# Kernel tuning notes

Hardware: AMD Instinct MI355X
Metric: run time of the kernel (lower is better)

Reference implementation:

```python
import jax, jax.numpy as jnp
import numpy as np

N = 100000       # nodes
E = 3200000      # edges
IN_DIM = 128
EDGE_DIM = 16
H = 64           # hidden_dim
L = 3            # num_layers
G = 256          # num graphs
BN_EPS = 1e-5


def setup_inputs() -> dict:
    key = jax.random.key(0)
    ks = jax.random.split(key, 16)
    x = jax.random.normal(ks[0], (N, IN_DIM), dtype=jnp.float32)
    edge_attr = jax.random.normal(ks[1], (E, EDGE_DIM), dtype=jnp.float32)
    edge_index = jax.random.randint(ks[2], (2, E), 0, N, dtype=jnp.int64)
    batch = jnp.sort(jax.random.randint(ks[3], (N,), 0, G, dtype=jnp.int64))
    s = 0.05
    np_w = jax.random.normal(ks[4], (IN_DIM, H), dtype=jnp.float32) * s
    np_b = jnp.zeros((H,), dtype=jnp.float32)
    ep_w = jax.random.normal(ks[5], (EDGE_DIM, H), dtype=jnp.float32) * s
    ep_b = jnp.zeros((H,), dtype=jnp.float32)
    mlp_w1 = jax.random.normal(ks[6], (L, H, H), dtype=jnp.float32) * s
    mlp_b1 = jnp.zeros((L, H), dtype=jnp.float32)
    mlp_w2 = jax.random.normal(ks[7], (L, H, H), dtype=jnp.float32) * s
    mlp_b2 = jnp.zeros((L, H), dtype=jnp.float32)
    bn_g = jnp.ones((L, H), dtype=jnp.float32)
    bn_b = jnp.zeros((L, H), dtype=jnp.float32)
    return {"x": x, "edge_attr": edge_attr, "edge_index": edge_index, "batch": batch,
            "np_w": np_w, "np_b": np_b, "ep_w": ep_w, "ep_b": ep_b,
            "mlp_w1": mlp_w1, "mlp_b1": mlp_b1, "mlp_w2": mlp_w2, "mlp_b2": mlp_b2,
            "bn_g": bn_g, "bn_b": bn_b}


def reference(x, edge_attr, edge_index, batch, np_w, np_b, ep_w, ep_b,
              mlp_w1, mlp_b1, mlp_w2, mlp_b2, bn_g, bn_b):
    h = x @ np_w + np_b                  # [N,H] node_proj
    e = edge_attr @ ep_w + ep_b          # [E,H] edge_proj
    src, dst = edge_index[0], edge_index[1]
    for l in range(L):
        # GINEConv (eps=0): MLP(x_i + sum_j ReLU(x_j + e_ij))
        msg = jax.nn.relu(h[src] + e)                          # [E,H] gather + edge add
        agg = jax.ops.segment_sum(msg, dst, num_segments=N)    # scatter-add
        z = h + agg
        z = jax.nn.relu(z @ mlp_w1[l] + mlp_b1[l]) @ mlp_w2[l] + mlp_b2[l]
        # BatchNorm1d over node dim (batch statistics, training-mode math)
        mu = jnp.mean(z, axis=0)
        var = jnp.mean((z - mu) ** 2, axis=0)
        z = (z - mu) * jax.lax.rsqrt(var + BN_EPS) * bn_g[l] + bn_b[l]
        h = jax.nn.relu(z)               # dropout omitted (deterministic reference)
    # global_mean_pool
    sums = jax.ops.segment_sum(h, batch, num_segments=G)
    cnts = jax.ops.segment_sum(jnp.ones((N,), dtype=h.dtype), batch, num_segments=G)
    graph_emb = sums / jnp.maximum(cnts, 1.0)[:, None]
    return h, graph_emb
```

## Files before the change

### kernel.cpp

```cpp
#include <hip/hip_runtime.h>
#include <hip/hip_bf16.h>

#define NN 100000
#define NE 3200000
#define IND 128
#define ED 16
#define HD 64
#define NL 3
#define NG 256
#define BN_EPS 1e-5f

#define NB 391
#define PBLK 512
#define PCHUNK 6250
#define MLP_BLOCKS 2048
#define APPLY_BLOCKS 2048

typedef unsigned int uint32;
typedef unsigned long long uint64;
typedef unsigned short ushort16;
typedef __attribute__((ext_vector_type(8))) short bf16x8;
typedef __attribute__((ext_vector_type(4))) float f32x4;

__device__ __forceinline__ ushort16 f2b(float f) {
    uint32 u = __float_as_uint(f);
    u = (u + 0x7fffu + ((u >> 16) & 1u)) >> 16;
    return (ushort16)u;
}
__device__ __forceinline__ float b2f(ushort16 b) {
    return __uint_as_float(((uint32)b) << 16);
}

__global__ __launch_bounds__(256) void k_node_proj(
    const float* __restrict__ x, const float* __restrict__ w,
    const float* __restrict__ b, ushort16* __restrict__ sb)
{
    __shared__ float xs[4][IND];
    const int wave = threadIdx.x >> 6, lane = threadIdx.x & 63;
    const int node = blockIdx.x * 4 + wave;
    const float2 v = *(const float2*)(x + (size_t)node * IND + lane * 2);
    ((float2*)xs[wave])[lane] = v;
    float acc = b[lane];
#pragma unroll
    for (int k = 0; k < IND; ++k)
        acc = fmaf(xs[wave][k], w[k * HD + lane], acc);
    sb[node * HD + lane] = f2b(acc);
}

__global__ __launch_bounds__(256) void k_p1(const int* __restrict__ ei,
                                            int* __restrict__ bh)
{
    __shared__ int hist[NB];
    const int t = threadIdx.x, blk = blockIdx.x;
    for (int i = t; i < NB; i += 256) hist[i] = 0;
    __syncthreads();
    const int base = blk * PCHUNK;
    for (int i = t; i < PCHUNK; i += 256)
        atomicAdd(&hist[ei[NE + base + i] >> 8], 1);
    __syncthreads();
    for (int i = t; i < NB; i += 256) bh[blk * NB + i] = hist[i];
}

__global__ __launch_bounds__(512) void k_p2(int* __restrict__ bh,
                                            int* __restrict__ bstart,
                                            int* __restrict__ rowptr)
{
    __shared__ int tot[NB];
    __shared__ int bsl[NB + 1];
    const int t = threadIdx.x;
    if (t < NB) {
        int s = 0;
        for (int blk = 0; blk < PBLK; ++blk) {
            const int idx = blk * NB + t;
            const int v = bh[idx];
            bh[idx] = s;
            s += v;
        }
        tot[t] = s;
    }
    __syncthreads();
    if (t == 0) {
        int run = 0;
        for (int b = 0; b < NB; ++b) { bsl[b] = run; run += tot[b]; }
        bsl[NB] = run;
    }
    __syncthreads();
    if (t < NB) {
        const int base = bsl[t];
        for (int blk = 0; blk < PBLK; ++blk) bh[blk * NB + t] += base;
        bstart[t] = base;
    }
    if (t == 0) { bstart[NB] = NE; rowptr[NN] = NE; }
}

__global__ __launch_bounds__(256) void k_p3(const int* __restrict__ ei,
                                            const int* __restrict__ bh,
                                            uint64* __restrict__ tmp)
{
    __shared__ int cursor[NB];
    const int t = threadIdx.x, blk = blockIdx.x;
    for (int i = t; i < NB; i += 256) cursor[i] = bh[blk * NB + i];
    __syncthreads();
    const int base = blk * PCHUNK;
    for (int i = t; i < PCHUNK; i += 256) {
        const int e = base + i;
        const int d = ei[NE + e];
        const int s = ei[e];
        const int pos = atomicAdd(&cursor[d >> 8], 1);
        tmp[pos] = (uint64)(uint32)d | ((uint64)(uint32)s << 17)
                 | ((uint64)(uint32)e << 34);
    }
}

__global__ __launch_bounds__(256) void k_p4(const uint64* __restrict__ tmp,
                                            const int* __restrict__ bstart,
                                            int* __restrict__ perm_src,
                                            int* __restrict__ perm_eid,
                                            int* __restrict__ rowptr)
{
    __shared__ int cnt[256], csave[256], cnt2[256];
    const int t = threadIdx.x, b = blockIdx.x;
    const int lo = bstart[b], hi = bstart[b + 1];
    cnt[t] = 0; cnt2[t] = 0;
    __syncthreads();
    for (int e = lo + t; e < hi; e += 256)
        atomicAdd(&cnt[(int)(tmp[e] & 0x1FFFF) & 255], 1);
    __syncthreads();
    csave[t] = cnt[t];
    __syncthreads();
    for (int off = 1; off < 256; off <<= 1) {
        const int v = (t >= off) ? cnt[t - off] : 0;
        __syncthreads();
        cnt[t] += v;
        __syncthreads();
    }
    const int excl = cnt[t] - csave[t];
    const int node = (b << 8) + t;
    if (node < NN) rowptr[node] = lo + excl;
    __syncthreads();
    csave[t] = excl;
    __syncthreads();
    for (int e = lo + t; e < hi; e += 256) {
        const uint64 u = tmp[e];
        const int loc = (int)(u & 0x1FFFF) & 255;
        const int r = atomicAdd(&cnt2[loc], 1);
        const int pos = lo + csave[loc] + r;
        perm_src[pos] = (int)((u >> 17) & 0x1FFFF);
        perm_eid[pos] = (int)(u >> 34);
    }
}

__global__ __launch_bounds__(256) void k_permute(
    const float* __restrict__ ea, const int* __restrict__ perm_eid,
    ushort16* __restrict__ ea_perm)
{
    const int pos = blockIdx.x * 256 + threadIdx.x;
    const int p = pos >> 2, q = pos & 3;
    const int eid = perm_eid[p];
    const float4 v = ((const float4*)(ea + (size_t)eid * ED))[q];
    ushort4 o;
    o.x = f2b(v.x); o.y = f2b(v.y); o.z = f2b(v.z); o.w = f2b(v.w);
    ((ushort4*)ea_perm)[pos] = o;
}

template <bool XFORM>
__global__ __launch_bounds__(256) void k_gather(
    const ushort16* __restrict__ eab, const int* __restrict__ perm_src,
    const int* __restrict__ rowptr,
    const float* __restrict__ epw, const float* __restrict__ epb,
    const ushort16* __restrict__ sb, const float* __restrict__ bnp,
    float* __restrict__ z)
{
    __shared__ float pe[4][64 * 17];
    const int lane = threadIdx.x & 63;
    const int wave = threadIdx.x >> 6;
    const int l15 = lane & 15, lg = lane >> 4;

    bf16x8 bfrag[4];
#pragma unroll
    for (int c = 0; c < 4; ++c) {
#pragma unroll
        for (int i = 0; i < 8; ++i) {
            const int k = lg * 8 + i;
            bfrag[c][i] = (k < ED) ? (short)f2b(epw[k * HD + c * 16 + l15])
                                   : (short)0;
        }
    }
    const float bc = epb[lane];
    const float tsc = XFORM ? bnp[lane] : 1.f;
    const float tsh = XFORM ? bnp[64 + lane] : 0.f;
    float* mype = pe[wave];

    const int node = __builtin_amdgcn_readfirstlane((blockIdx.x << 2) + wave);
    const int rs = rowptr[node];
    const int re = rowptr[node + 1];

    float acc = 0.f;
    for (int j = rs; j < re; j += 16) {
        bf16x8 a = {};
        if (lg < 2) {
            int row = j + l15;
            if (row > NE - 1) row = NE - 1;
            a = *(const bf16x8*)((const short*)eab + (size_t)row * ED + lg * 8);
        }
        const f32x4 zero = {0.f, 0.f, 0.f, 0.f};
#pragma unroll
        for (int c = 0; c < 4; ++c) {
            const f32x4 d = __builtin_amdgcn_mfma_f32_16x16x32_bf16(
                a, bfrag[c], zero, 0, 0, 0);
            const int base = (c * 16 + l15) * 17 + lg * 4;
#pragma unroll
            for (int v = 0; v < 4; ++v) mype[base + v] = d[v];
        }
#pragma unroll
        for (int half = 0; half < 2; ++half) {
            const int jb = j + half * 8;
            int s[8];
#pragma unroll
            for (int m = 0; m < 8; ++m) {
                int idx = jb + m;
                if (idx > NE - 1) idx = NE - 1;
                s[m] = perm_src[idx];
            }
            float hv[8];
#pragma unroll
            for (int m = 0; m < 8; ++m) {
                float v = b2f(sb[(size_t)s[m] * HD + lane]);
                if (XFORM) v = fmaxf(fmaf(v, tsc, tsh), 0.f);
                hv[m] = v;
            }
            const int lim = re - jb;
#pragma unroll
            for (int m = 0; m < 8; ++m) {
                if (m < lim) {
                    const float e = mype[lane * 17 + half * 8 + m] + bc;
                    acc += fmaxf(hv[m] + e, 0.f);
                }
            }
        }
    }
    float u0 = b2f(sb[(size_t)node * HD + lane]);
    if (XFORM) u0 = fmaxf(fmaf(u0, tsc, tsh), 0.f);
    z[node * HD + lane] = acc + u0;
}

template <bool STORE_BF16>
__global__ __launch_bounds__(256) void k_mlp(
    float* __restrict__ z,
    const float* __restrict__ w1, const float* __restrict__ b1,
    const float* __restrict__ w2, const float* __restrict__ b2,
    ushort16* __restrict__ sb, float* __restrict__ part)
{
    __shared__ float z0s[4][HD];
    __shared__ float t1s[4][HD];
    __shared__ float red[4][2][HD];
    const int wave = threadIdx.x >> 6, lane = threadIdx.x & 63;
    const float vb1 = b1[lane], vb2 = b2[lane];
    float s1 = 0.f, s2 = 0.f;
    for (int node = blockIdx.x * 4 + wave; node < NN; node += MLP_BLOCKS * 4) {
        const int idx = node * HD + lane;
        z0s[wave][lane] = z[idx];
        float a = vb1;
#pragma unroll
        for (int k = 0; k < HD; ++k)
            a = fmaf(z0s[wave][k], w1[k * HD + lane], a);
        a = fmaxf(a, 0.f);
        t1s[wave][lane] = a;
        float o = vb2;
#pragma unroll
        for (int k = 0; k < HD; ++k)
            o = fmaf(t1s[wave][k], w2[k * HD + lane], o);
        if (STORE_BF16) sb[idx] = f2b(o);
        else            z[idx] = o;
        s1 += o;
        s2 += o * o;
    }
    red[wave][0][lane] = s1;
    red[wave][1][lane] = s2;
    __syncthreads();
    if (wave == 0) {
        float a = red[0][0][lane] + red[1][0][lane] + red[2][0][lane] + red[3][0][lane];
        float c = red[0][1][lane] + red[1][1][lane] + red[2][1][lane] + red[3][1][lane];
        part[blockIdx.x * 128 + lane] = a;
        part[blockIdx.x * 128 + 64 + lane] = c;
    }
}

__global__ __launch_bounds__(1024) void k_bn_final(
    const float* __restrict__ part,
    const float* __restrict__ g, const float* __restrict__ b,
    float* __restrict__ bnp)
{
    __shared__ float red[16][2][HD];
    const int c = threadIdx.x & 63;
    const int s = threadIdx.x >> 6;
    float s1 = 0.f, s2 = 0.f;
    for (int i = s; i < MLP_BLOCKS; i += 16) {
        s1 += part[i * 128 + c];
        s2 += part[i * 128 + 64 + c];
    }
    red[s][0][c] = s1;
    red[s][1][c] = s2;
    __syncthreads();
    if (s == 0) {
        float a = 0.f, q = 0.f;
#pragma unroll
        for (int i = 0; i < 16; ++i) { a += red[i][0][c]; q += red[i][1][c]; }
        const float mu  = a / (float)NN;
        const float var = q / (float)NN - mu * mu;
        const float rstd = rsqrtf(var + BN_EPS);
        const float sc = rstd * g[c];
        bnp[c] = sc;
        bnp[64 + c] = b[c] - mu * sc;
    }
}

__global__ __launch_bounds__(256) void k_bn_apply(
    const float* __restrict__ t2, const float* __restrict__ bnp,
    float* __restrict__ h)
{
    const int lane = threadIdx.x & 63;
    const float sc = bnp[lane];
    const float sh = bnp[64 + lane];
    int i = blockIdx.x * 256 + threadIdx.x;
    const int stride = APPLY_BLOCKS * 256;
    for (; i < NN * HD; i += stride)
        h[i] = fmaxf(t2[i] * sc + sh, 0.f);
}

__global__ __launch_bounds__(256) void k_pool(
    const float* __restrict__ h, const int* __restrict__ batch,
    float* __restrict__ emb)
{
    __shared__ float red[4][HD];
    const int g = blockIdx.x;
    const int lane = threadIdx.x & 63;
    const int wave = threadIdx.x >> 6;
    int lo = 0, hi = NN;
    while (lo < hi) { int m = (lo + hi) >> 1; if (batch[m] < g) lo = m + 1; else hi = m; }
    const int start = lo;
    hi = NN;
    while (lo < hi) { int m = (lo + hi) >> 1; if (batch[m] <= g) lo = m + 1; else hi = m; }
    const int end = lo;
    float acc = 0.f;
    for (int n = start + wave; n < end; n += 4) acc += h[(size_t)n * HD + lane];
    red[wave][lane] = acc;
    __syncthreads();
    if (wave == 0) {
        float a = red[0][lane] + red[1][lane] + red[2][lane] + red[3][lane];
        emb[g * HD + lane] = a / fmaxf((float)(end - start), 1.f);
    }
}

extern "C" void kernel_launch(void* const* d_in, const int* in_sizes, int n_in,
                              void* d_out, int out_size, void* d_ws, size_t ws_size,
                              hipStream_t stream)
{
    const float* x     = (const float*)d_in[0];
    const float* ea    = (const float*)d_in[1];
    const int*   ei    = (const int*)d_in[2];
    const int*   batch = (const int*)d_in[3];
    const float* np_w  = (const float*)d_in[4];
    const float* np_b  = (const float*)d_in[5];
    const float* ep_w  = (const float*)d_in[6];
    const float* ep_b  = (const float*)d_in[7];
    const float* w1    = (const float*)d_in[8];
    const float* b1    = (const float*)d_in[9];
    const float* w2    = (const float*)d_in[10];
    const float* b2    = (const float*)d_in[11];
    const float* bng   = (const float*)d_in[12];
    const float* bnb   = (const float*)d_in[13];

    float* h   = (float*)d_out;
    float* emb = h + (size_t)NN * HD;

    char* ws = (char*)d_ws;
    float*     agg      = (float*)    (ws);
    uint64*    tmp      = (uint64*)   (ws);
    float*     part     = (float*)    (ws + 25600000);
    float*     bnp      = (float*)    (ws + 26648576);
    int*       bh       = (int*)      (ws + 26650112);
    int*       bstart   = (int*)      (ws + 27450880);
    int*       rowptr   = (int*)      (ws + 27452448);
    ushort16*  sb       = (ushort16*) (ws + 27852464);
    int*       perm_src = (int*)      (ws + 40652464);
    int*       perm_eid = (int*)      (ws + 53452464);
    ushort16*  ea_perm  = (ushort16*) (ws + 66252464);

    k_node_proj<<<NN / 4, 256, 0, stream>>>(x, np_w, np_b, sb);

    k_p1<<<PBLK, 256, 0, stream>>>(ei, bh);
    k_p2<<<1, 512, 0, stream>>>(bh, bstart, rowptr);
    k_p3<<<PBLK, 256, 0, stream>>>(ei, bh, tmp);
    k_p4<<<NB, 256, 0, stream>>>(tmp, bstart, perm_src, perm_eid, rowptr);
    k_permute<<<NE * 4 / 256, 256, 0, stream>>>(ea, perm_eid, ea_perm);

    for (int l = 0; l < NL; ++l) {
        if (l == 0)
            k_gather<false><<<NN / 4, 256, 0, stream>>>(
                ea_perm, perm_src, rowptr, ep_w, ep_b, sb, bnp, agg);
        else
            k_gather<true><<<NN / 4, 256, 0, stream>>>(
                ea_perm, perm_src, rowptr, ep_w, ep_b, sb, bnp + (l - 1) * 128, agg);
        if (l < NL - 1)
            k_mlp<true><<<MLP_BLOCKS, 256, 0, stream>>>(
                agg, w1 + l * HD * HD, b1 + l * HD, w2 + l * HD * HD, b2 + l * HD,
                sb, part);
        else
            k_mlp<false><<<MLP_BLOCKS, 256, 0, stream>>>(
                agg, w1 + l * HD * HD, b1 + l * HD, w2 + l * HD * HD, b2 + l * HD,
                sb, part);
        k_bn_final<<<1, 1024, 0, stream>>>(part, bng + l * HD, bnb + l * HD, bnp + l * 128);
    }

    k_bn_apply<<<APPLY_BLOCKS, 256, 0, stream>>>(agg, bnp + 2 * 128, h);
    k_pool<<<NG, 256, 0, stream>>>(h, batch, emb);
}
```

Baseline: 1.301 ms.

## Prefetch 16 neighbor gathers before MFMA and fold edge bias into matmul

In the gather kernel, all 16 source indices and neighbor features are now loaded up front, before the edge-projection MFMA, so the gather latency overlaps with the matrix work instead of being issued in two serialized halves. The edge bias is folded into the MFMA by adding a constant-one column to the A fragment and a bias row to the B fragment, which drops a per-edge add. MLP_BLOCKS is also reduced from 2048 to 512. Holding 16 gathered values live raises register pressure, and the bias is now rounded to bf16.

```diff
diff --git a/kernel.cpp b/kernel.cpp
--- a/kernel.cpp
+++ b/kernel.cpp
@@ -13,7 +13,7 @@
 #define NB 391
 #define PBLK 512
 #define PCHUNK 6250
-#define MLP_BLOCKS 2048
+#define MLP_BLOCKS 512
 #define APPLY_BLOCKS 2048
 
 typedef unsigned int uint32;
@@ -182,11 +182,12 @@
 #pragma unroll
         for (int i = 0; i < 8; ++i) {
             const int k = lg * 8 + i;
-            bfrag[c][i] = (k < ED) ? (short)f2b(epw[k * HD + c * 16 + l15])
-                                   : (short)0;
-        }
-    }
-    const float bc = epb[lane];
+            short v = 0;
+            if (k < ED)       v = (short)f2b(epw[k * HD + c * 16 + l15]);
+            else if (k == ED) v = (short)f2b(epb[c * 16 + l15]);
+            bfrag[c][i] = v;
+        }
+    }
     const float tsc = XFORM ? bnp[lane] : 1.f;
     const float tsh = XFORM ? bnp[64 + lane] : 0.f;
     float* mype = pe[wave];
@@ -197,12 +198,27 @@
 
     float acc = 0.f;
     for (int j = rs; j < re; j += 16) {
+        int s[16];
+#pragma unroll
+        for (int m = 0; m < 16; ++m) {
+            int idx = j + m;
+            if (idx > NE - 1) idx = NE - 1;
+            s[m] = perm_src[idx];
+        }
+        float hv[16];
+#pragma unroll
+        for (int m = 0; m < 16; ++m)
+            hv[m] = b2f(sb[(size_t)s[m] * HD + lane]);
+
         bf16x8 a = {};
         if (lg < 2) {
             int row = j + l15;
             if (row > NE - 1) row = NE - 1;
             a = *(const bf16x8*)((const short*)eab + (size_t)row * ED + lg * 8);
-        }
+        } else if (lg == 2) {
+            a[0] = (short)0x3F80;
+        }
+
         const f32x4 zero = {0.f, 0.f, 0.f, 0.f};
 #pragma unroll
         for (int c = 0; c < 4; ++c) {
@@ -212,31 +228,17 @@
 #pragma unroll
             for (int v = 0; v < 4; ++v) mype[base + v] = d[v];
         }
-#pragma unroll
-        for (int half = 0; half < 2; ++half) {
-            const int jb = j + half * 8;
-            int s[8];
-#pragma unroll
-            for (int m = 0; m < 8; ++m) {
-                int idx = jb + m;
-                if (idx > NE - 1) idx = NE - 1;
-                s[m] = perm_src[idx];
-            }
-            float hv[8];
-#pragma unroll
-            for (int m = 0; m < 8; ++m) {
-                float v = b2f(sb[(size_t)s[m] * HD + lane]);
-                if (XFORM) v = fmaxf(fmaf(v, tsc, tsh), 0.f);
-                hv[m] = v;
-            }
-            const int lim = re - jb;
-#pragma unroll
-            for (int m = 0; m < 8; ++m) {
-                if (m < lim) {
-                    const float e = mype[lane * 17 + half * 8 + m] + bc;
-                    acc += fmaxf(hv[m] + e, 0.f);
-                }
-            }
+
+        if (XFORM) {
+#pragma unroll
+            for (int m = 0; m < 16; ++m)
+                hv[m] = fmaxf(fmaf(hv[m], tsc, tsh), 0.f);
+        }
+        const int lim = re - j;
+#pragma unroll
+        for (int m = 0; m < 16; ++m) {
+            if (m < lim)
+                acc += fmaxf(hv[m] + mype[lane * 17 + m], 0.f);
         }
     }
     float u0 = b2f(sb[(size_t)node * HD + lane]);
```

Result: faster. 1.217 ms (-6.4%).
